# Kernel tuning notes

Hardware: AMD Instinct MI355X
Metric: run time of the kernel (lower is better)

The kernel has to match this reference:

```python
import jax, jax.numpy as jnp
import numpy as np

NPOINT = 2048
NSAMPLE = 16
LEAKY = 0.1
BN_EPS = 1e-5


def square_distance(src, dst):
    # src [B,S,3], dst [B,N,3] -> [B,S,N] squared euclidean
    d = -2.0 * jnp.einsum('bsc,bnc->bsn', src, dst)
    d = d + jnp.sum(src * src, -1)[:, :, None]
    d = d + jnp.sum(dst * dst, -1)[:, None, :]
    return d


def furthest_point_sample(xyz, npoint):
    # xyz [B,N,3] -> idx [B,npoint]; matches pointnet2 CUDA (seed = index 0)
    B, N, _ = xyz.shape

    def step(carry, _):
        dist, far = carry  # dist [B,N], far [B]
        centroid = jnp.take_along_axis(xyz, far[:, None, None], axis=1)  # [B,1,3]
        d = jnp.sum((xyz - centroid) ** 2, axis=-1)
        dist = jnp.minimum(dist, d)
        nxt = jnp.argmax(dist, axis=-1).astype(jnp.int32)
        return (dist, nxt), far

    init = (jnp.full((B, N), 1e10, xyz.dtype), jnp.zeros((B,), jnp.int32))
    _, idxs = jax.lax.scan(step, init, None, length=npoint)
    return idxs.T  # [B, npoint]


def _gather_nbrs(p, i):
    # p [N,C], i [S,K] -> [S,K,C]
    return p[i]


gather_group = jax.vmap(_gather_nbrs)


def conv_bn_lrelu(x, W, g, b):
    # x [B,Cin,S,K], W [Cout,Cin]; 1x1 conv + train-mode BatchNorm2d + LeakyReLU
    y = jnp.einsum('oc,bcsk->bosk', W, x)
    mean = jnp.mean(y, axis=(0, 2, 3), keepdims=True)
    var = jnp.var(y, axis=(0, 2, 3), keepdims=True)
    y = (y - mean) * jax.lax.rsqrt(var + BN_EPS)
    y = y * g[None, :, None, None] + b[None, :, None, None]
    return jnp.where(y > 0, y, LEAKY * y)


def setup_inputs() -> dict:
    key = jax.random.key(0)
    ks = jax.random.split(key, 5)
    B, N, D = 4, 8192, 64
    return {
        'xyz': jax.random.normal(ks[0], (B, 3, N), jnp.float32),
        'points': jax.random.normal(ks[1], (B, D, N), jnp.float32),
        'conv0_w': jax.random.normal(ks[2], (64, 67), jnp.float32) * 0.05,
        'conv1_w': jax.random.normal(ks[3], (64, 64), jnp.float32) * 0.05,
        'conv2_w': jax.random.normal(ks[4], (128, 64), jnp.float32) * 0.05,
        'bn0_g': jnp.ones((64,), jnp.float32),
        'bn0_b': jnp.zeros((64,), jnp.float32),
        'bn1_g': jnp.ones((64,), jnp.float32),
        'bn1_b': jnp.zeros((64,), jnp.float32),
        'bn2_g': jnp.ones((128,), jnp.float32),
        'bn2_b': jnp.zeros((128,), jnp.float32),
    }


def reference(xyz, points, conv0_w, conv1_w, conv2_w,
              bn0_g, bn0_b, bn1_g, bn1_b, bn2_g, bn2_b):
    xyz_t = jnp.transpose(xyz, (0, 2, 1))      # [B,N,3]
    pts_t = jnp.transpose(points, (0, 2, 1))   # [B,N,D]

    fps_idx = furthest_point_sample(xyz_t, NPOINT)                       # [B,S]
    new_xyz = jnp.take_along_axis(xyz_t, fps_idx[:, :, None], axis=1)    # [B,S,3]

    sqrd = square_distance(new_xyz, xyz_t)                               # [B,S,N]
    _, idx = jax.lax.top_k(-sqrd, NSAMPLE)                               # [B,S,K]

    grouped_xyz = gather_group(xyz_t, idx)                               # [B,S,K,3]
    grouped_norm = grouped_xyz - new_xyz[:, :, None, :]
    grouped_pts = gather_group(pts_t, idx)                               # [B,S,K,D]
    new_points = jnp.concatenate([grouped_norm, grouped_pts], axis=-1)   # [B,S,K,D+3]
    new_points = jnp.transpose(new_points, (0, 3, 1, 2))                 # [B,D+3,S,K]

    for W, g, b in ((conv0_w, bn0_g, bn0_b), (conv1_w, bn1_g, bn1_b),
                    (conv2_w, bn2_g, bn2_b)):
        new_points = conv_bn_lrelu(new_points, W, g, b)

    feat = jnp.max(new_points, axis=-1)                                  # [B,128,S]
    return jnp.transpose(new_xyz, (0, 2, 1)), feat, fps_idx
```

## Files before the change

### kernel.cpp

```cpp
#include <hip/hip_runtime.h>
#include <hip/hip_bf16.h>

#define BB 4
#define NP 8192
#define SS 2048
#define KK 16
#define DD 64
#define NN (BB*SS*KK)

__device__ __forceinline__ float wave_max_f32(float v) {
  int x;
  x = __builtin_amdgcn_update_dpp(0, __float_as_int(v), 0xB1, 0xF, 0xF, true);
  v = fmaxf(v, __int_as_float(x));
  x = __builtin_amdgcn_update_dpp(0, __float_as_int(v), 0x4E, 0xF, 0xF, true);
  v = fmaxf(v, __int_as_float(x));
  x = __builtin_amdgcn_update_dpp(0, __float_as_int(v), 0x141, 0xF, 0xF, true);
  v = fmaxf(v, __int_as_float(x));
  x = __builtin_amdgcn_update_dpp(0, __float_as_int(v), 0x140, 0xF, 0xF, true);
  v = fmaxf(v, __int_as_float(x));
  x = __builtin_amdgcn_ds_swizzle(__float_as_int(v), 0x401F);
  v = fmaxf(v, __int_as_float(x));
  v = fmaxf(v, __shfl_xor(v, 32, 64));
  return v;
}

__global__ __launch_bounds__(512) void fps_kernel(
    const float* __restrict__ xyz, float* __restrict__ newXyz,
    float* __restrict__ out)
{
  const int b = blockIdx.x;
  const int t = threadIdx.x;
  const float* xb = xyz + (size_t)b * 3 * NP;

  __shared__ float lx[NP], ly[NP], lz[NP];
  __shared__ int   wis[SS];
  __shared__ unsigned long long swin[3];

  float px[16], py[16], pz[16], dist[16];
#pragma unroll
  for (int j = 0; j < 16; j++) {
    int i = t + (j << 9);
    float x = xb[i], y = xb[NP + i], z = xb[2 * NP + i];
    px[j] = x; py[j] = y; pz[j] = z; dist[j] = 1e10f;
    lx[i] = x; ly[i] = y; lz[i] = z;
  }
  if (t == 0) { wis[0] = 0; swin[0] = 0; swin[1] = 0; swin[2] = 0; }
  __syncthreads();

  float cx = lx[0], cy = ly[0], cz = lz[0];

  for (int it = 1; it < SS; ++it) {
    float lbest = -1.0f;
#pragma unroll
    for (int j = 0; j < 16; j++) {
      float dx = __fsub_rn(px[j], cx);
      float dy = __fsub_rn(py[j], cy);
      float dz = __fsub_rn(pz[j], cz);
      float d = __fadd_rn(__fadd_rn(__fmul_rn(dx, dx), __fmul_rn(dy, dy)), __fmul_rn(dz, dz));
      float dm = fminf(dist[j], d);
      dist[j] = dm;
      lbest = fmaxf(lbest, dm);
    }
    float Vw = wave_max_f32(lbest);
    int q = it % 3;
    if (lbest == Vw) {
      unsigned mi = 0u;
#pragma unroll
      for (int j = 15; j >= 0; j--) {
        if (dist[j] == Vw) mi = (unsigned)(t + (j << 9));
      }
      unsigned long long pk =
          ((unsigned long long)__float_as_uint(Vw) << 32) | (unsigned)(~mi);
      atomicMax(&swin[q], pk);
    }
    __syncthreads();
    unsigned long long pkf = swin[q];
    int ii = (int)(~((unsigned)pkf));
    if (t == 0) { wis[it] = ii; swin[(q + 2) % 3] = 0; }
    cx = lx[ii]; cy = ly[ii]; cz = lz[ii];
  }
  __syncthreads();

  float* outX = out;
  float* outI = out + 24576 + 1048576;
  for (int s = t; s < SS; s += 512) {
    int iw = wis[s];
    float x = lx[iw], y = ly[iw], z = lz[iw];
    size_t qq = (size_t)(b * SS + s);
    newXyz[qq * 3 + 0] = x;
    newXyz[qq * 3 + 1] = y;
    newXyz[qq * 3 + 2] = z;
    outX[(b * 3 + 0) * SS + s] = x;
    outX[(b * 3 + 1) * SS + s] = y;
    outX[(b * 3 + 2) * SS + s] = z;
    outI[b * SS + s] = (float)iw;
  }
}

__global__ __launch_bounds__(256) void knn_kernel(
    const float* __restrict__ xyz, const float* __restrict__ newXyz,
    int* __restrict__ knnIdx)
{
  const int t = threadIdx.x, w = t >> 6, l = t & 63;
  const int q = blockIdx.x * 4 + w;
  const int b = q >> 11;
  const float* xb = xyz + (size_t)b * 3 * NP;
  float qx = newXyz[q * 3], qy = newXyz[q * 3 + 1], qz = newXyz[q * 3 + 2];
  float ss = __fadd_rn(__fadd_rn(__fmul_rn(qx, qx), __fmul_rn(qy, qy)), __fmul_rn(qz, qz));
  float kd[16]; int ki[16];
#pragma unroll
  for (int j = 0; j < 16; j++) { kd[j] = __builtin_inff(); ki[j] = 0x7fffffff; }

  for (int m = 0; m < 128; m++) {
    int i = l + (m << 6);
    float x = xb[i], y = xb[NP + i], z = xb[2 * NP + i];
    float dot = __fadd_rn(__fadd_rn(__fmul_rn(x, qx), __fmul_rn(y, qy)), __fmul_rn(z, qz));
    float nn  = __fadd_rn(__fadd_rn(__fmul_rn(x, x), __fmul_rn(y, y)), __fmul_rn(z, z));
    float d   = __fadd_rn(__fadd_rn(__fmul_rn(-2.0f, dot), ss), nn);
    if (d < kd[15]) {
      kd[15] = d; ki[15] = i;
#pragma unroll
      for (int jj = 15; jj >= 1; jj--) {
        if (kd[jj] < kd[jj - 1]) {
          float td = kd[jj]; kd[jj] = kd[jj - 1]; kd[jj - 1] = td;
          int   ti = ki[jj]; ki[jj] = ki[jj - 1]; ki[jj - 1] = ti;
        }
      }
    }
  }

  __shared__ float sd[4 * 64 * 17];
  __shared__ int   sx[4 * 64 * 17];
  int base = (w * 64 + l) * 17;
#pragma unroll
  for (int j = 0; j < 16; j++) { sd[base + j] = kd[j]; sx[base + j] = ki[j]; }
  __syncthreads();

  int cur = 0; int outIdx = 0;
#pragma unroll 1
  for (int r = 0; r < 16; r++) {
    float hv = (cur < 16) ? sd[base + cur] : __builtin_inff();
    int   hi = (cur < 16) ? sx[base + cur] : 0x7fffffff;
    int   hl = l;
#pragma unroll
    for (int m2 = 1; m2 < 64; m2 <<= 1) {
      float ov = __shfl_xor(hv, m2, 64);
      int   oi = __shfl_xor(hi, m2, 64);
      int   ol = __shfl_xor(hl, m2, 64);
      if (ov < hv || (ov == hv && oi < hi)) { hv = ov; hi = oi; hl = ol; }
    }
    if (l == hl) cur++;
    if (l == r) outIdx = hi;
  }
  if (l < 16) knnIdx[q * 16 + l] = outIdx;
}

__global__ __launch_bounds__(256) void build_x0(
    const float* __restrict__ xyz, const float* __restrict__ points,
    const float* __restrict__ newXyz, const int* __restrict__ knnIdx,
    float* __restrict__ X)
{
  int n = blockIdx.x * 256 + threadIdx.x;
  int b = n >> 15;
  int q = n >> 4;
  int ip = knnIdx[n];
  const float* xb = xyz + (size_t)b * 3 * NP;
  X[(size_t)0 * NN + n] = xb[ip]          - newXyz[q * 3 + 0];
  X[(size_t)1 * NN + n] = xb[NP + ip]     - newXyz[q * 3 + 1];
  X[(size_t)2 * NN + n] = xb[2 * NP + ip] - newXyz[q * 3 + 2];
  const float* pb = points + (size_t)b * DD * NP;
#pragma unroll 8
  for (int d0 = 0; d0 < DD; d0++)
    X[(size_t)(3 + d0) * NN + n] = pb[(size_t)d0 * NP + ip];
}

template <int CIN, int COUT>
__global__ __launch_bounds__(256) void conv_kernel(
    const float* __restrict__ X, const float* __restrict__ W, float* __restrict__ Y)
{
  int n = blockIdx.x * 256 + threadIdx.x;
  float x[CIN];
#pragma unroll
  for (int c = 0; c < CIN; c++) x[c] = X[(size_t)c * NN + n];
#pragma unroll 1
  for (int o = 0; o < COUT; o += 4) {
    float a0 = 0.f, a1 = 0.f, a2 = 0.f, a3 = 0.f;
#pragma unroll
    for (int c = 0; c < CIN; c++) {
      float xv = x[c];
      a0 = fmaf(W[(o + 0) * CIN + c], xv, a0);
      a1 = fmaf(W[(o + 1) * CIN + c], xv, a1);
      a2 = fmaf(W[(o + 2) * CIN + c], xv, a2);
      a3 = fmaf(W[(o + 3) * CIN + c], xv, a3);
    }
    Y[(size_t)(o + 0) * NN + n] = a0;
    Y[(size_t)(o + 1) * NN + n] = a1;
    Y[(size_t)(o + 2) * NN + n] = a2;
    Y[(size_t)(o + 3) * NN + n] = a3;
  }
}

__global__ __launch_bounds__(256) void stats_kernel(
    const float* __restrict__ Y, float* __restrict__ stats)
{
  int c = blockIdx.y;
  int base = blockIdx.x * 4096 + threadIdx.x;
  const float* yc = Y + (size_t)c * NN;
  float s1 = 0.f, s2 = 0.f;
#pragma unroll
  for (int j = 0; j < 16; j++) {
    float v = yc[base + j * 256];
    s1 += v; s2 = fmaf(v, v, s2);
  }
#pragma unroll
  for (int m = 1; m < 64; m <<= 1) {
    s1 += __shfl_xor(s1, m, 64);
    s2 += __shfl_xor(s2, m, 64);
  }
  __shared__ float r1[4], r2[4];
  int w = threadIdx.x >> 6;
  if ((threadIdx.x & 63) == 0) { r1[w] = s1; r2[w] = s2; }
  __syncthreads();
  if (threadIdx.x == 0) {
    float t1 = r1[0] + r1[1] + r1[2] + r1[3];
    float t2 = r2[0] + r2[1] + r2[2] + r2[3];
    atomicAdd(&stats[c * 2], t1);
    atomicAdd(&stats[c * 2 + 1], t2);
  }
}

__global__ __launch_bounds__(256) void bn_lrelu_kernel(
    float* __restrict__ Y, const float* __restrict__ stats,
    const float* __restrict__ g, const float* __restrict__ bt)
{
  int c = blockIdx.y;
  int n = blockIdx.x * 256 + threadIdx.x;
  float mean = stats[c * 2] * (1.0f / NN);
  float var  = stats[c * 2 + 1] * (1.0f / NN) - mean * mean;
  float inv  = rsqrtf(var + 1e-5f);
  float gamma = g[c], beta = bt[c];
  size_t o = (size_t)c * NN + n;
  float v = (Y[o] - mean) * inv;
  v = v * gamma + beta;
  Y[o] = v > 0.0f ? v : 0.1f * v;
}

__global__ __launch_bounds__(256) void maxk_kernel(
    const float* __restrict__ X, float* __restrict__ out)
{
  int m = blockIdx.x * 256 + threadIdx.x;
  int s = m & 2047;
  int o = (m >> 11) & 127;
  int b = m >> 18;
  const float4* p = (const float4*)(X + (size_t)o * NN + ((size_t)((b << 11) + s) << 4));
  float4 v0 = p[0], v1 = p[1], v2 = p[2], v3 = p[3];
  float mx = fmaxf(fmaxf(fmaxf(v0.x, v0.y), fmaxf(v0.z, v0.w)),
                   fmaxf(fmaxf(v1.x, v1.y), fmaxf(v1.z, v1.w)));
  mx = fmaxf(mx, fmaxf(fmaxf(fmaxf(v2.x, v2.y), fmaxf(v2.z, v2.w)),
                       fmaxf(fmaxf(v3.x, v3.y), fmaxf(v3.z, v3.w))));
  out[24576 + (size_t)((b << 7) + o) * SS + s] = mx;
}

extern "C" void kernel_launch(void* const* d_in, const int* in_sizes, int n_in,
                              void* d_out, int out_size, void* d_ws, size_t ws_size,
                              hipStream_t stream) {
  const float* xyz    = (const float*)d_in[0];
  const float* points = (const float*)d_in[1];
  const float* w0 = (const float*)d_in[2];
  const float* w1 = (const float*)d_in[3];
  const float* w2 = (const float*)d_in[4];
  const float* g0 = (const float*)d_in[5];
  const float* b0 = (const float*)d_in[6];
  const float* g1 = (const float*)d_in[7];
  const float* b1 = (const float*)d_in[8];
  const float* g2 = (const float*)d_in[9];
  const float* b2 = (const float*)d_in[10];
  float* out = (float*)d_out;

  float* wsf    = (float*)d_ws;
  float* newXyz = wsf;
  int*   knnIdx = (int*)(wsf + 24576);
  float* stats  = wsf + 155648;
  float* Xa     = wsf + 155904;
  float* Xb     = wsf + 8937728;

  fps_kernel<<<BB, 512, 0, stream>>>(xyz, newXyz, out);
  knn_kernel<<<SS * BB / 4, 256, 0, stream>>>(xyz, newXyz, knnIdx);
  build_x0<<<NN / 256, 256, 0, stream>>>(xyz, points, newXyz, knnIdx, Xa);

  hipMemsetAsync(stats, 0, 256 * 4, stream);
  conv_kernel<67, 64><<<NN / 256, 256, 0, stream>>>(Xa, w0, Xb);
  stats_kernel<<<dim3(32, 64), 256, 0, stream>>>(Xb, stats);
  bn_lrelu_kernel<<<dim3(NN / 256, 64), 256, 0, stream>>>(Xb, stats, g0, b0);

  hipMemsetAsync(stats, 0, 256 * 4, stream);
  conv_kernel<64, 64><<<NN / 256, 256, 0, stream>>>(Xb, w1, Xa);
  stats_kernel<<<dim3(32, 64), 256, 0, stream>>>(Xa, stats);
  bn_lrelu_kernel<<<dim3(NN / 256, 64), 256, 0, stream>>>(Xa, stats, g1, b1);

  hipMemsetAsync(stats, 0, 256 * 4, stream);
  conv_kernel<64, 128><<<NN / 256, 256, 0, stream>>>(Xa, w2, Xb);
  stats_kernel<<<dim3(32, 128), 256, 0, stream>>>(Xb, stats);
  bn_lrelu_kernel<<<dim3(NN / 256, 128), 256, 0, stream>>>(Xb, stats, g2, b2);

  maxk_kernel<<<(BB * 128 * SS) / 256, 256, 0, stream>>>(Xb, out);
}
```

Measured before the change: 2.735 ms.

## Fold BN+LeakyReLU into next conv/maxk and pack FPS into float2 math

Removes the standalone bn_lrelu passes. A tiny finalize kernel now turns the accumulated statistics into a per-channel scale and shift, which the following conv applies as it loads its inputs and maxk applies before its reduction. This avoids a full read-modify-write of each activation tensor. Separately, FPS runs with 256 threads, each holding two points per slot as float2 vectors so the compiler can use packed FP32 ops, with contraction disabled to keep rounding identical.

```diff
diff --git a/kernel.cpp b/kernel.cpp
--- a/kernel.cpp
+++ b/kernel.cpp
@@ -8,6 +8,8 @@
 #define DD 64
 #define NN (BB*SS*KK)
 
+typedef float vf2 __attribute__((ext_vector_type(2)));
+
 __device__ __forceinline__ float wave_max_f32(float v) {
   int x;
   x = __builtin_amdgcn_update_dpp(0, __float_as_int(v), 0xB1, 0xF, 0xF, true);
@@ -24,7 +26,7 @@
   return v;
 }
 
-__global__ __launch_bounds__(512) void fps_kernel(
+__global__ __launch_bounds__(256) void fps_kernel(
     const float* __restrict__ xyz, float* __restrict__ newXyz,
     float* __restrict__ out)
 {
@@ -36,13 +38,16 @@
   __shared__ int   wis[SS];
   __shared__ unsigned long long swin[3];
 
-  float px[16], py[16], pz[16], dist[16];
+  vf2 px[16], py[16], pz[16], dist[16];
 #pragma unroll
   for (int j = 0; j < 16; j++) {
-    int i = t + (j << 9);
-    float x = xb[i], y = xb[NP + i], z = xb[2 * NP + i];
-    px[j] = x; py[j] = y; pz[j] = z; dist[j] = 1e10f;
-    lx[i] = x; ly[i] = y; lz[i] = z;
+    int i = (j << 9) + (t << 1);
+    vf2 x = *(const vf2*)(xb + i);
+    vf2 y = *(const vf2*)(xb + NP + i);
+    vf2 z = *(const vf2*)(xb + 2 * NP + i);
+    px[j] = x; py[j] = y; pz[j] = z;
+    dist[j] = (vf2){1e10f, 1e10f};
+    *(vf2*)(lx + i) = x; *(vf2*)(ly + i) = y; *(vf2*)(lz + i) = z;
   }
   if (t == 0) { wis[0] = 0; swin[0] = 0; swin[1] = 0; swin[2] = 0; }
   __syncthreads();
@@ -50,24 +55,31 @@
   float cx = lx[0], cy = ly[0], cz = lz[0];
 
   for (int it = 1; it < SS; ++it) {
-    float lbest = -1.0f;
-#pragma unroll
-    for (int j = 0; j < 16; j++) {
-      float dx = __fsub_rn(px[j], cx);
-      float dy = __fsub_rn(py[j], cy);
-      float dz = __fsub_rn(pz[j], cz);
-      float d = __fadd_rn(__fadd_rn(__fmul_rn(dx, dx), __fmul_rn(dy, dy)), __fmul_rn(dz, dz));
-      float dm = fminf(dist[j], d);
-      dist[j] = dm;
-      lbest = fmaxf(lbest, dm);
-    }
+    vf2 c2x = {cx, cx}, c2y = {cy, cy}, c2z = {cz, cz};
+    vf2 lb = {-1.0f, -1.0f};
+    {
+#pragma clang fp contract(off)
+#pragma unroll
+      for (int j = 0; j < 16; j++) {
+        vf2 dx = px[j] - c2x;
+        vf2 dy = py[j] - c2y;
+        vf2 dz = pz[j] - c2z;
+        vf2 d  = (dx * dx + dy * dy) + dz * dz;
+        vf2 dm = __builtin_elementwise_min(dist[j], d);
+        dist[j] = dm;
+        lb = __builtin_elementwise_max(lb, dm);
+      }
+    }
+    float lbest = fmaxf(lb.x, lb.y);
     float Vw = wave_max_f32(lbest);
     int q = it % 3;
     if (lbest == Vw) {
       unsigned mi = 0u;
 #pragma unroll
       for (int j = 15; j >= 0; j--) {
-        if (dist[j] == Vw) mi = (unsigned)(t + (j << 9));
+        unsigned base = (unsigned)((j << 9) + (t << 1));
+        if (dist[j].y == Vw) mi = base + 1;
+        if (dist[j].x == Vw) mi = base;
       }
       unsigned long long pk =
           ((unsigned long long)__float_as_uint(Vw) << 32) | (unsigned)(~mi);
@@ -83,7 +95,7 @@
 
   float* outX = out;
   float* outI = out + 24576 + 1048576;
-  for (int s = t; s < SS; s += 512) {
+  for (int s = t; s < SS; s += 256) {
     int iw = wis[s];
     float x = lx[iw], y = ly[iw], z = lz[iw];
     size_t qq = (size_t)(b * SS + s);
@@ -174,14 +186,28 @@
     X[(size_t)(3 + d0) * NN + n] = pb[(size_t)d0 * NP + ip];
 }
 
-template <int CIN, int COUT>
+template <int CIN, int COUT, bool BNIN>
 __global__ __launch_bounds__(256) void conv_kernel(
-    const float* __restrict__ X, const float* __restrict__ W, float* __restrict__ Y)
-{
+    const float* __restrict__ X, const float* __restrict__ W,
+    const float* __restrict__ ss, float* __restrict__ Y)
+{
+  __shared__ vf2 sss[CIN];
+  if (BNIN) {
+    for (int i = threadIdx.x; i < CIN; i += 256) sss[i] = ((const vf2*)ss)[i];
+    __syncthreads();
+  }
   int n = blockIdx.x * 256 + threadIdx.x;
   float x[CIN];
 #pragma unroll
   for (int c = 0; c < CIN; c++) x[c] = X[(size_t)c * NN + n];
+  if (BNIN) {
+#pragma unroll
+    for (int c = 0; c < CIN; c++) {
+      vf2 p = sss[c];
+      float v = fmaf(x[c], p.x, p.y);
+      x[c] = v > 0.0f ? v : 0.1f * v;
+    }
+  }
 #pragma unroll 1
   for (int o = 0; o < COUT; o += 4) {
     float a0 = 0.f, a1 = 0.f, a2 = 0.f, a3 = 0.f;
@@ -229,35 +255,43 @@
   }
 }
 
-__global__ __launch_bounds__(256) void bn_lrelu_kernel(
-    float* __restrict__ Y, const float* __restrict__ stats,
-    const float* __restrict__ g, const float* __restrict__ bt)
-{
-  int c = blockIdx.y;
-  int n = blockIdx.x * 256 + threadIdx.x;
-  float mean = stats[c * 2] * (1.0f / NN);
-  float var  = stats[c * 2 + 1] * (1.0f / NN) - mean * mean;
-  float inv  = rsqrtf(var + 1e-5f);
-  float gamma = g[c], beta = bt[c];
-  size_t o = (size_t)c * NN + n;
-  float v = (Y[o] - mean) * inv;
-  v = v * gamma + beta;
-  Y[o] = v > 0.0f ? v : 0.1f * v;
+template <int C>
+__global__ void finalize_kernel(const float* __restrict__ stats,
+                                const float* __restrict__ g,
+                                const float* __restrict__ bt,
+                                float* __restrict__ ss)
+{
+  int c = threadIdx.x;
+  if (c < C) {
+    float mean = stats[c * 2] * (1.0f / NN);
+    float var  = stats[c * 2 + 1] * (1.0f / NN) - mean * mean;
+    float inv  = rsqrtf(var + 1e-5f);
+    float sc = inv * g[c];
+    float sh = bt[c] - mean * sc;
+    ss[c * 2] = sc; ss[c * 2 + 1] = sh;
+  }
 }
 
 __global__ __launch_bounds__(256) void maxk_kernel(
-    const float* __restrict__ X, float* __restrict__ out)
+    const float* __restrict__ X, const float* __restrict__ ss,
+    float* __restrict__ out)
 {
   int m = blockIdx.x * 256 + threadIdx.x;
   int s = m & 2047;
   int o = (m >> 11) & 127;
   int b = m >> 18;
+  float sc = ss[2 * o], sh = ss[2 * o + 1];
   const float4* p = (const float4*)(X + (size_t)o * NN + ((size_t)((b << 11) + s) << 4));
-  float4 v0 = p[0], v1 = p[1], v2 = p[2], v3 = p[3];
-  float mx = fmaxf(fmaxf(fmaxf(v0.x, v0.y), fmaxf(v0.z, v0.w)),
-                   fmaxf(fmaxf(v1.x, v1.y), fmaxf(v1.z, v1.w)));
-  mx = fmaxf(mx, fmaxf(fmaxf(fmaxf(v2.x, v2.y), fmaxf(v2.z, v2.w)),
-                       fmaxf(fmaxf(v3.x, v3.y), fmaxf(v3.z, v3.w))));
+  float mx = -__builtin_inff();
+#pragma unroll
+  for (int j = 0; j < 4; j++) {
+    float4 v4 = p[j];
+    float a = fmaf(v4.x, sc, sh); a = a > 0.f ? a : 0.1f * a;
+    float b2 = fmaf(v4.y, sc, sh); b2 = b2 > 0.f ? b2 : 0.1f * b2;
+    float c = fmaf(v4.z, sc, sh); c = c > 0.f ? c : 0.1f * c;
+    float d = fmaf(v4.w, sc, sh); d = d > 0.f ? d : 0.1f * d;
+    mx = fmaxf(mx, fmaxf(fmaxf(a, b2), fmaxf(c, d)));
+  }
   out[24576 + (size_t)((b << 7) + o) * SS + s] = mx;
 }
 
@@ -280,28 +314,32 @@
   float* wsf    = (float*)d_ws;
   float* newXyz = wsf;
   int*   knnIdx = (int*)(wsf + 24576);
-  float* stats  = wsf + 155648;
-  float* Xa     = wsf + 155904;
-  float* Xb     = wsf + 8937728;
-
-  fps_kernel<<<BB, 512, 0, stream>>>(xyz, newXyz, out);
+  float* stats0 = wsf + 155648;
+  float* stats1 = wsf + 155904;
+  float* stats2 = wsf + 156160;
+  float* ss0    = wsf + 156416;
+  float* ss1    = wsf + 156672;
+  float* ss2    = wsf + 156928;
+  float* Xa     = wsf + 160000;
+  float* Xb     = wsf + 8941824;
+
+  fps_kernel<<<BB, 256, 0, stream>>>(xyz, newXyz, out);
   knn_kernel<<<SS * BB / 4, 256, 0, stream>>>(xyz, newXyz, knnIdx);
   build_x0<<<NN / 256, 256, 0, stream>>>(xyz, points, newXyz, knnIdx, Xa);
 
-  hipMemsetAsync(stats, 0, 256 * 4, stream);
-  conv_kernel<67, 64><<<NN / 256, 256, 0, stream>>>(Xa, w0, Xb);
-  stats_kernel<<<dim3(32, 64), 256, 0, stream>>>(Xb, stats);
-  bn_lrelu_kernel<<<dim3(NN / 256, 64), 256, 0, stream>>>(Xb, stats, g0, b0);
-
-  hipMemsetAsync(stats, 0, 256 * 4, stream);
-  conv_kernel<64, 64><<<NN / 256, 256, 0, stream>>>(Xb, w1, Xa);
-  stats_kernel<<<dim3(32, 64), 256, 0, stream>>>(Xa, stats);
-  bn_lrelu_kernel<<<dim3(NN / 256, 64), 256, 0, stream>>>(Xa, stats, g1, b1);
-
-  hipMemsetAsync(stats, 0, 256 * 4, stream);
-  conv_kernel<64, 128><<<NN / 256, 256, 0, stream>>>(Xa, w2, Xb);
-  stats_kernel<<<dim3(32, 128), 256, 0, stream>>>(Xb, stats);
-  bn_lrelu_kernel<<<dim3(NN / 256, 128), 256, 0, stream>>>(Xb, stats, g2, b2);
-
-  maxk_kernel<<<(BB * 128 * SS) / 256, 256, 0, stream>>>(Xb, out);
-}
+  hipMemsetAsync(stats0, 0, 1536 * 4, stream);
+
+  conv_kernel<67, 64, false><<<NN / 256, 256, 0, stream>>>(Xa, w0, nullptr, Xb);
+  stats_kernel<<<dim3(32, 64), 256, 0, stream>>>(Xb, stats0);
+  finalize_kernel<64><<<1, 128, 0, stream>>>(stats0, g0, b0, ss0);
+
+  conv_kernel<64, 64, true><<<NN / 256, 256, 0, stream>>>(Xb, w1, ss0, Xa);
+  stats_kernel<<<dim3(32, 64), 256, 0, stream>>>(Xa, stats1);
+  finalize_kernel<64><<<1, 128, 0, stream>>>(stats1, g1, b1, ss1);
+
+  conv_kernel<64, 128, true><<<NN / 256, 256, 0, stream>>>(Xa, w2, ss1, Xb);
+  stats_kernel<<<dim3(32, 128), 256, 0, stream>>>(Xb, stats2);
+  finalize_kernel<128><<<1, 128, 0, stream>>>(stats2, g2, b2, ss2);
+
+  maxk_kernel<<<(BB * 128 * SS) / 256, 256, 0, stream>>>(Xb, ss2, out);
+}
```

Result: slower. 2.937 ms (+7.4%).
